# Optimization experiments

Measured on AMD Instinct MI355X. Metric: run time of the kernel, lower is better.

## Reference

```python
import jax, jax.numpy as jnp
import numpy as np

N_NODES = 100000
N_REL = 500
N_EDGES = 600000
DIM = 128


def setup_inputs() -> dict:
    key = jax.random.key(0)
    ks = jax.random.split(key, 10)
    ent = jax.random.normal(ks[0], (N_NODES, DIM), dtype=jnp.float32)
    rel = jax.random.normal(ks[1], (N_REL, DIM), dtype=jnp.float32)
    edge_index = jax.random.randint(ks[2], (2, N_EDGES), 0, N_NODES, dtype=jnp.int64)
    edge_type = jax.random.randint(ks[3], (N_EDGES,), 0, N_REL, dtype=jnp.int64)
    s = 1.0 / np.sqrt(DIM)
    W_self = jax.random.uniform(ks[4], (DIM, DIM), jnp.float32, -s, s)
    b_self = jax.random.uniform(ks[5], (DIM,), jnp.float32, -s, s)
    W_nei = jax.random.uniform(ks[6], (DIM, DIM), jnp.float32, -s, s)
    b_nei = jax.random.uniform(ks[7], (DIM,), jnp.float32, -s, s)
    W_rel = jax.random.uniform(ks[8], (DIM, DIM), jnp.float32, -s, s)
    b_rel = jax.random.uniform(ks[9], (DIM,), jnp.float32, -s, s)
    return {
        "ent": ent, "rel": rel, "edge_index": edge_index, "edge_type": edge_type,
        "W_self": W_self, "b_self": b_self,
        "W_nei": W_nei, "b_nei": b_nei,
        "W_rel": W_rel, "b_rel": b_rel,
    }


def reference(ent, rel, edge_index, edge_type, W_self, b_self, W_nei, b_nei, W_rel, b_rel):
    src, dst = edge_index[0], edge_index[1]
    # gather -> sigmoid-gate -> scatter-add
    msg = ent[src] * jax.nn.sigmoid(rel[edge_type])          # [E, dim]
    agg = jax.ops.segment_sum(msg, dst, num_segments=ent.shape[0])  # [N, dim]
    out_ent = jax.nn.relu(ent @ W_self.T + b_self + agg @ W_nei.T + b_nei)
    out_rel = rel @ W_rel.T + b_rel
    return (out_ent, out_rel)
```

## Files before the change

kernel.cpp:

```cpp
#include <hip/hip_runtime.h>
#include <hip/hip_bf16.h>
#include <math.h>

#define DIM 128

typedef __bf16 bf8 __attribute__((ext_vector_type(8)));
typedef float f4 __attribute__((ext_vector_type(4)));

struct __align__(8) bf16x4 { __hip_bfloat162 a, b; };

__global__ __launch_bounds__(256) void prep_kernel(
    const float* __restrict__ rel,
    const float* __restrict__ Ws,
    const float* __restrict__ Wn,
    const float* __restrict__ Wr,
    __hip_bfloat16* __restrict__ sigb,
    __hip_bfloat16* __restrict__ Wcat,
    float* __restrict__ Wt_rel,
    int* __restrict__ offs,
    int nSig, int sigBlocks, int N) {
    int b = blockIdx.x;
    if (b < sigBlocks) {
        int i = b * 256 + threadIdx.x;
        if (i < nSig) {
            float x = rel[i];
            sigb[i] = __float2bfloat16(1.0f / (1.0f + expf(-x)));
        }
    } else if (b < sigBlocks + 32) {
        int idx = (b - sigBlocks) * 256 + threadIdx.x;
        int j  = idx >> 6;
        int k0 = (idx & 63) * 4;
        const float* src = (k0 < DIM) ? &Ws[j * DIM + k0] : &Wn[j * DIM + (k0 - DIM)];
        float4 v = *(const float4*)src;
        bf16x4 o;
        o.a.x = __float2bfloat16(v.x);
        o.a.y = __float2bfloat16(v.y);
        o.b.x = __float2bfloat16(v.z);
        o.b.y = __float2bfloat16(v.w);
        *(bf16x4*)&Wcat[(size_t)j * 256 + k0] = o;
    } else if (b < sigBlocks + 32 + 64) {
        int id = (b - sigBlocks - 32) * 256 + threadIdx.x;
        int k = id >> 7;
        int j = id & 127;
        Wt_rel[id] = Wr[j * DIM + k];
    } else {
        int i = (b - sigBlocks - 32 - 64) * 256 + threadIdx.x;
        if (i <= N) offs[i] = 0;
    }
}

__global__ __launch_bounds__(256) void conv_hist_kernel(
    const float* __restrict__ ent,
    __hip_bfloat16* __restrict__ xcat,
    const int* __restrict__ edge_index,
    int* __restrict__ counts,
    int* __restrict__ rank,
    int N, int E, int convBlocks) {
    if ((int)blockIdx.x < convBlocks) {
        long long tid = (long long)blockIdx.x * 256 + threadIdx.x;
        int row = (int)(tid >> 5);
        int q   = (int)(tid & 31);
        if (row >= N) return;
        float4 v = *(const float4*)&ent[(size_t)row * DIM + q * 4];
        bf16x4 o;
        o.a.x = __float2bfloat16(v.x);
        o.a.y = __float2bfloat16(v.y);
        o.b.x = __float2bfloat16(v.z);
        o.b.y = __float2bfloat16(v.w);
        *(bf16x4*)&xcat[(size_t)row * 256 + q * 4] = o;
    } else {
        int e = (blockIdx.x - convBlocks) * 256 + threadIdx.x;
        if (e < E) {
            rank[e] = atomicAdd(&counts[edge_index[E + e]], 1);
        }
    }
}

#define SCAN_TPB 256
#define SCAN_IPT 4
#define SCAN_IPB 1024

__global__ void scan_pass1(int* __restrict__ data,
                           int* __restrict__ blockSums, int N) {
    __shared__ int ts[SCAN_TPB];
    int t = threadIdx.x;
    int base = blockIdx.x * SCAN_IPB + t * SCAN_IPT;
    int v[SCAN_IPT];
    int s = 0;
    #pragma unroll
    for (int i = 0; i < SCAN_IPT; ++i) {
        int idx = base + i;
        v[i] = (idx < N) ? data[idx] : 0;
        s += v[i];
    }
    ts[t] = s;
    __syncthreads();
    for (int off = 1; off < SCAN_TPB; off <<= 1) {
        int x = (t >= off) ? ts[t - off] : 0;
        __syncthreads();
        ts[t] += x;
        __syncthreads();
    }
    int excl = ts[t] - s;
    #pragma unroll
    for (int i = 0; i < SCAN_IPT; ++i) {
        int idx = base + i;
        if (idx < N) data[idx] = excl;
        excl += v[i];
    }
    if (t == SCAN_TPB - 1) blockSums[blockIdx.x] = ts[t];
}

__global__ __launch_bounds__(256) void scan_finish_kernel(
    int* __restrict__ offs, const int* __restrict__ blockSums,
    int nb, int N, int E) {
    __shared__ int ps[128];
    __shared__ int eps[128];
    int t = threadIdx.x;
    int v = 0;
    if (t < 128) {
        v = (t < nb) ? blockSums[t] : 0;
        ps[t] = v;
    }
    __syncthreads();
    for (int off = 1; off < 128; off <<= 1) {
        int x = (t >= off && t < 128) ? ps[t - off] : 0;
        __syncthreads();
        if (t < 128) ps[t] += x;
        __syncthreads();
    }
    if (t < 128) eps[t] = ps[t] - v;
    __syncthreads();
    int i = blockIdx.x * 256 + t;
    if (i < N)  offs[i] += eps[i >> 10];
    if (i == N) offs[N] = E;
}

__global__ void scatter_ids_kernel(const int* __restrict__ edge_index,
                                   const int* __restrict__ edge_type,
                                   const int* __restrict__ offs,
                                   const int* __restrict__ rank,
                                   unsigned* __restrict__ spack, int E) {
    int e = blockIdx.x * blockDim.x + threadIdx.x;
    if (e >= E) return;
    int dst = edge_index[E + e];
    int p = offs[dst] + rank[e];
    spack[p] = (unsigned)edge_index[e] | ((unsigned)edge_type[e] << 17);
}

__global__ __launch_bounds__(256) void agg_relout_kernel(
    const __hip_bfloat16* __restrict__ xcat,
    const __hip_bfloat16* __restrict__ sigb,
    const int* __restrict__ offs,
    const unsigned* __restrict__ spack,
    __hip_bfloat16* __restrict__ xcat_w,
    const float* __restrict__ rel,
    const float* __restrict__ Wt_rel,
    const float* __restrict__ b_rel,
    float* __restrict__ out_rel,
    int N, int R, int aggBlocks) {
    if ((int)blockIdx.x < aggBlocks) {
        int wid  = (int)((blockIdx.x * (long long)256 + threadIdx.x) >> 6);
        int lane = threadIdx.x & 63;
        if (wid >= N) return;
        int beg = offs[wid], end = offs[wid + 1];
        float ax0 = 0.f, ay0 = 0.f, ax1 = 0.f, ay1 = 0.f;
        for (int e = beg; e < end; e += 4) {
            int r = end - e;
            unsigned p0 = spack[e];
            unsigned p1 = spack[r > 1 ? e + 1 : e];
            unsigned p2 = spack[r > 2 ? e + 2 : e];
            unsigned p3 = spack[r > 3 ? e + 3 : e];
            __hip_bfloat162 v0 = *(const __hip_bfloat162*)&xcat[(size_t)(p0 & 0x1FFFFu) * 256 + lane * 2];
            __hip_bfloat162 v1 = *(const __hip_bfloat162*)&xcat[(size_t)(p1 & 0x1FFFFu) * 256 + lane * 2];
            __hip_bfloat162 v2 = *(const __hip_bfloat162*)&xcat[(size_t)(p2 & 0x1FFFFu) * 256 + lane * 2];
            __hip_bfloat162 v3 = *(const __hip_bfloat162*)&xcat[(size_t)(p3 & 0x1FFFFu) * 256 + lane * 2];
            __hip_bfloat162 g0 = *(const __hip_bfloat162*)&sigb[(size_t)(p0 >> 17) * DIM + lane * 2];
            __hip_bfloat162 g1 = *(const __hip_bfloat162*)&sigb[(size_t)(p1 >> 17) * DIM + lane * 2];
            __hip_bfloat162 g2 = *(const __hip_bfloat162*)&sigb[(size_t)(p2 >> 17) * DIM + lane * 2];
            __hip_bfloat162 g3 = *(const __hip_bfloat162*)&sigb[(size_t)(p3 >> 17) * DIM + lane * 2];
            float m1 = (r > 1) ? 1.f : 0.f;
            float m2 = (r > 2) ? 1.f : 0.f;
            float m3 = (r > 3) ? 1.f : 0.f;
            ax0 += __bfloat162float(v0.x) * __bfloat162float(g0.x);
            ay0 += __bfloat162float(v0.y) * __bfloat162float(g0.y);
            ax1 += m1 * (__bfloat162float(v1.x) * __bfloat162float(g1.x));
            ay1 += m1 * (__bfloat162float(v1.y) * __bfloat162float(g1.y));
            ax0 += m2 * (__bfloat162float(v2.x) * __bfloat162float(g2.x));
            ay0 += m2 * (__bfloat162float(v2.y) * __bfloat162float(g2.y));
            ax1 += m3 * (__bfloat162float(v3.x) * __bfloat162float(g3.x));
            ay1 += m3 * (__bfloat162float(v3.y) * __bfloat162float(g3.y));
        }
        __hip_bfloat162 o;
        o.x = __float2bfloat16(ax0 + ax1);
        o.y = __float2bfloat16(ay0 + ay1);
        *(__hip_bfloat162*)&xcat_w[(size_t)wid * 256 + 128 + lane * 2] = o;
    } else {
        __shared__ float rr[2][DIM];
        int idx  = blockIdx.x - aggBlocks;
        int half = threadIdx.x >> 7;
        int col  = threadIdx.x & 127;
        int row  = idx * 2 + half;
        if (row < R) rr[half][col] = rel[(size_t)row * DIM + col];
        __syncthreads();
        if (row >= R) return;
        float acc = b_rel[col];
        #pragma unroll 8
        for (int k = 0; k < DIM; ++k) {
            acc += rr[half][k] * Wt_rel[k * DIM + col];
        }
        out_rel[(size_t)row * DIM + col] = acc;
    }
}

__global__ __launch_bounds__(256) void gemm_mfma_kernel(
    const __hip_bfloat16* xcat,
    const __hip_bfloat16* __restrict__ Wcat,
    const float* __restrict__ b_self,
    const float* __restrict__ b_nei,
    float* out, int N) {
    __shared__ __hip_bfloat16 Bs[128][264];

    int t    = threadIdx.x;
    int wave = t >> 6;
    int lane = t & 63;
    int quad = lane >> 4;
    int r16  = lane & 15;

    {
        int r = t >> 1, h = t & 1;
        const float4* src = (const float4*)&Wcat[(size_t)r * 256 + h * 128];
        #pragma unroll
        for (int i = 0; i < 16; ++i) {
            *(float4*)&Bs[r][h * 128 + i * 8] = src[i];
        }
    }
    __syncthreads();

    int row0 = blockIdx.x * 128 + wave * 32;

    bf8 x[2][8];
    #pragma unroll
    for (int mt = 0; mt < 2; ++mt) {
        int m = row0 + mt * 16 + r16;
        if (m > N - 1) m = N - 1;
        const __hip_bfloat16* xp = &xcat[(size_t)m * 256 + quad * 8];
        #pragma unroll
        for (int ks = 0; ks < 8; ++ks) {
            x[mt][ks] = *(const bf8*)(xp + ks * 32);
        }
    }

    f4 acc[2][8];
    #pragma unroll
    for (int mt = 0; mt < 2; ++mt)
        #pragma unroll
        for (int jt = 0; jt < 8; ++jt)
            acc[mt][jt] = (f4){0.f, 0.f, 0.f, 0.f};

    #pragma unroll
    for (int ks = 0; ks < 8; ++ks) {
        #pragma unroll
        for (int jt = 0; jt < 8; ++jt) {
            bf8 w = *(const bf8*)&Bs[jt * 16 + r16][ks * 32 + quad * 8];
            acc[0][jt] = __builtin_amdgcn_mfma_f32_16x16x32_bf16(w, x[0][ks], acc[0][jt], 0, 0, 0);
            acc[1][jt] = __builtin_amdgcn_mfma_f32_16x16x32_bf16(w, x[1][ks], acc[1][jt], 0, 0, 0);
        }
    }

    f4 bias4[8];
    #pragma unroll
    for (int jt = 0; jt < 8; ++jt) {
        const float4 bs = *(const float4*)&b_self[jt * 16 + quad * 4];
        const float4 bn = *(const float4*)&b_nei[jt * 16 + quad * 4];
        bias4[jt] = (f4){bs.x + bn.x, bs.y + bn.y, bs.z + bn.z, bs.w + bn.w};
    }

    #pragma unroll
    for (int mt = 0; mt < 2; ++mt) {
        int m = row0 + mt * 16 + r16;
        if (m < N) {
            #pragma unroll
            for (int jt = 0; jt < 8; ++jt) {
                f4 v = acc[mt][jt] + bias4[jt];
                float4 o;
                o.x = fmaxf(v[0], 0.f);
                o.y = fmaxf(v[1], 0.f);
                o.z = fmaxf(v[2], 0.f);
                o.w = fmaxf(v[3], 0.f);
                *(float4*)&out[(size_t)m * DIM + jt * 16 + quad * 4] = o;
            }
        }
    }
}

extern "C" void kernel_launch(void* const* d_in, const int* in_sizes, int n_in,
                              void* d_out, int out_size, void* d_ws, size_t ws_size,
                              hipStream_t stream) {
    const float* ent        = (const float*)d_in[0];
    const float* rel        = (const float*)d_in[1];
    const int*   edge_index = (const int*)d_in[2];
    const int*   edge_type  = (const int*)d_in[3];
    const float* W_self     = (const float*)d_in[4];
    const float* b_self     = (const float*)d_in[5];
    const float* W_nei      = (const float*)d_in[6];
    const float* b_nei      = (const float*)d_in[7];
    const float* W_rel      = (const float*)d_in[8];
    const float* b_rel      = (const float*)d_in[9];

    const int N = in_sizes[0] / DIM;
    const int R = in_sizes[1] / DIM;
    const int E = in_sizes[3];

    float* out     = (float*)d_out;
    float* out_rel = out + (size_t)N * DIM;
    __hip_bfloat16* xcat = (__hip_bfloat16*)d_out;

    __hip_bfloat16* sigb = (__hip_bfloat16*)d_ws;
    float* Wt_rel  = (float*)(sigb + (size_t)R * DIM);
    __hip_bfloat16* Wcat = (__hip_bfloat16*)(Wt_rel + DIM * DIM);
    int*   offs    = (int*)(Wcat + 128 * 256);
    int*   bsums   = offs + (N + 8);
    int*   rank    = bsums + 128;
    unsigned* spack = (unsigned*)(rank + E);

    const int nSig = R * DIM;
    const int sigBlocks = (nSig + 255) / 256;
    const int zeroBlocks = (N + 1 + 255) / 256;
    const int scanBlocks = (N + SCAN_IPB - 1) / SCAN_IPB;

    prep_kernel<<<sigBlocks + 32 + 64 + zeroBlocks, 256, 0, stream>>>(
        rel, W_self, W_nei, W_rel, sigb, Wcat, Wt_rel, offs, nSig, sigBlocks, N);

    {
        int convBlocks = (int)(((long long)N * 32 + 255) / 256);
        int histBlocks = (E + 255) / 256;
        conv_hist_kernel<<<convBlocks + histBlocks, 256, 0, stream>>>(
            ent, xcat, edge_index, offs, rank, N, E, convBlocks);
    }

    scan_pass1<<<scanBlocks, SCAN_TPB, 0, stream>>>(offs, bsums, N);
    scan_finish_kernel<<<(N + 1 + 255) / 256, 256, 0, stream>>>(
        offs, bsums, scanBlocks, N, E);

    scatter_ids_kernel<<<(E + 255) / 256, 256, 0, stream>>>(
        edge_index, edge_type, offs, rank, spack, E);

    {
        int aggBlocks = (int)(((long long)N * 64 + 255) / 256);
        int relBlocks = (R + 1) / 2;
        agg_relout_kernel<<<aggBlocks + relBlocks, 256, 0, stream>>>(
            xcat, sigb, offs, spack, xcat, rel, Wt_rel, b_rel, out_rel,
            N, R, aggBlocks);
    }

    {
        int blocks = (N + 127) / 128;
        gemm_mfma_kernel<<<blocks, 256, 0, stream>>>(xcat, Wcat, b_self, b_nei, out, N);
    }
}
```

Before: 227.1 us.

## Split wavefront into two edge groups with vectorized index loads and fp32 gates

```diff
diff --git a/kernel.cpp b/kernel.cpp
--- a/kernel.cpp
+++ b/kernel.cpp
@@ -14,17 +14,21 @@
     const float* __restrict__ Ws,
     const float* __restrict__ Wn,
     const float* __restrict__ Wr,
-    __hip_bfloat16* __restrict__ sigb,
+    float* __restrict__ sigf,
     __hip_bfloat16* __restrict__ Wcat,
     float* __restrict__ Wt_rel,
     int* __restrict__ offs,
-    int nSig, int sigBlocks, int N) {
+    int nSig, int nSigTot, int sigBlocks, int N) {
     int b = blockIdx.x;
     if (b < sigBlocks) {
         int i = b * 256 + threadIdx.x;
-        if (i < nSig) {
-            float x = rel[i];
-            sigb[i] = __float2bfloat16(1.0f / (1.0f + expf(-x)));
+        if (i < nSigTot) {
+            float v = 0.f;
+            if (i < nSig) {
+                float x = rel[i];
+                v = 1.0f / (1.0f + expf(-x));
+            }
+            sigf[i] = v;
         }
     } else if (b < sigBlocks + 32) {
         int idx = (b - sigBlocks) * 256 + threadIdx.x;
@@ -150,7 +154,7 @@
 
 __global__ __launch_bounds__(256) void agg_relout_kernel(
     const __hip_bfloat16* __restrict__ xcat,
-    const __hip_bfloat16* __restrict__ sigb,
+    const float* __restrict__ sigf,
     const int* __restrict__ offs,
     const unsigned* __restrict__ spack,
     __hip_bfloat16* __restrict__ xcat_w,
@@ -163,38 +167,47 @@
         int wid  = (int)((blockIdx.x * (long long)256 + threadIdx.x) >> 6);
         int lane = threadIdx.x & 63;
         if (wid >= N) return;
+        int h = lane >> 5;
+        int s = lane & 31;
         int beg = offs[wid], end = offs[wid + 1];
-        float ax0 = 0.f, ay0 = 0.f, ax1 = 0.f, ay1 = 0.f;
-        for (int e = beg; e < end; e += 4) {
-            int r = end - e;
-            unsigned p0 = spack[e];
-            unsigned p1 = spack[r > 1 ? e + 1 : e];
-            unsigned p2 = spack[r > 2 ? e + 2 : e];
-            unsigned p3 = spack[r > 3 ? e + 3 : e];
-            __hip_bfloat162 v0 = *(const __hip_bfloat162*)&xcat[(size_t)(p0 & 0x1FFFFu) * 256 + lane * 2];
-            __hip_bfloat162 v1 = *(const __hip_bfloat162*)&xcat[(size_t)(p1 & 0x1FFFFu) * 256 + lane * 2];
-            __hip_bfloat162 v2 = *(const __hip_bfloat162*)&xcat[(size_t)(p2 & 0x1FFFFu) * 256 + lane * 2];
-            __hip_bfloat162 v3 = *(const __hip_bfloat162*)&xcat[(size_t)(p3 & 0x1FFFFu) * 256 + lane * 2];
-            __hip_bfloat162 g0 = *(const __hip_bfloat162*)&sigb[(size_t)(p0 >> 17) * DIM + lane * 2];
-            __hip_bfloat162 g1 = *(const __hip_bfloat162*)&sigb[(size_t)(p1 >> 17) * DIM + lane * 2];
-            __hip_bfloat162 g2 = *(const __hip_bfloat162*)&sigb[(size_t)(p2 >> 17) * DIM + lane * 2];
-            __hip_bfloat162 g3 = *(const __hip_bfloat162*)&sigb[(size_t)(p3 >> 17) * DIM + lane * 2];
-            float m1 = (r > 1) ? 1.f : 0.f;
-            float m2 = (r > 2) ? 1.f : 0.f;
-            float m3 = (r > 3) ? 1.f : 0.f;
-            ax0 += __bfloat162float(v0.x) * __bfloat162float(g0.x);
-            ay0 += __bfloat162float(v0.y) * __bfloat162float(g0.y);
-            ax1 += m1 * (__bfloat162float(v1.x) * __bfloat162float(g1.x));
-            ay1 += m1 * (__bfloat162float(v1.y) * __bfloat162float(g1.y));
-            ax0 += m2 * (__bfloat162float(v2.x) * __bfloat162float(g2.x));
-            ay0 += m2 * (__bfloat162float(v2.y) * __bfloat162float(g2.y));
-            ax1 += m3 * (__bfloat162float(v3.x) * __bfloat162float(g3.x));
-            ay1 += m3 * (__bfloat162float(v3.y) * __bfloat162float(g3.y));
-        }
-        __hip_bfloat162 o;
-        o.x = __float2bfloat16(ax0 + ax1);
-        o.y = __float2bfloat16(ay0 + ay1);
-        *(__hip_bfloat162*)&xcat_w[(size_t)wid * 256 + 128 + lane * 2] = o;
+        unsigned len = (unsigned)(end - beg);
+        const unsigned SENT = ((unsigned)R) << 17;
+        unsigned so8  = (unsigned)s * 8;
+        unsigned so16 = (unsigned)s * 16;
+        float a0 = 0.f, a1 = 0.f, a2 = 0.f, a3 = 0.f;
+        int e0 = beg & ~3;
+        for (int e = e0; e < end; e += 8) {
+            int i0 = e + 4 * h;
+            uint4 pp = *(const uint4*)&spack[i0];
+            unsigned o0 = (unsigned)(i0 - beg);
+            unsigned p0 = (o0     < len) ? pp.x : SENT;
+            unsigned p1 = (o0 + 1 < len) ? pp.y : SENT;
+            unsigned p2 = (o0 + 2 < len) ? pp.z : SENT;
+            unsigned p3 = (o0 + 3 < len) ? pp.w : SENT;
+            #define EDGE(pj) { \
+                unsigned rb = (pj & 0x1FFFFu) << 9; \
+                unsigned tb = (pj >> 17) << 9; \
+                bf16x4 v = *(const bf16x4*)((const char*)xcat + rb + so8); \
+                float4 g = *(const float4*)((const char*)sigf + tb + so16); \
+                a0 += __bfloat162float(v.a.x) * g.x; \
+                a1 += __bfloat162float(v.a.y) * g.y; \
+                a2 += __bfloat162float(v.b.x) * g.z; \
+                a3 += __bfloat162float(v.b.y) * g.w; }
+            EDGE(p0); EDGE(p1); EDGE(p2); EDGE(p3);
+            #undef EDGE
+        }
+        a0 += __shfl_xor(a0, 32);
+        a1 += __shfl_xor(a1, 32);
+        a2 += __shfl_xor(a2, 32);
+        a3 += __shfl_xor(a3, 32);
+        if (h == 0) {
+            bf16x4 o;
+            o.a.x = __float2bfloat16(a0);
+            o.a.y = __float2bfloat16(a1);
+            o.b.x = __float2bfloat16(a2);
+            o.b.y = __float2bfloat16(a3);
+            *(bf16x4*)&xcat_w[(size_t)wid * 256 + 128 + s * 4] = o;
+        }
     } else {
         __shared__ float rr[2][DIM];
         int idx  = blockIdx.x - aggBlocks;
@@ -316,21 +329,23 @@
     float* out_rel = out + (size_t)N * DIM;
     __hip_bfloat16* xcat = (__hip_bfloat16*)d_out;
 
-    __hip_bfloat16* sigb = (__hip_bfloat16*)d_ws;
-    float* Wt_rel  = (float*)(sigb + (size_t)R * DIM);
+    float* sigf = (float*)d_ws;
+    float* Wt_rel  = sigf + (size_t)(R + 1) * DIM;
     __hip_bfloat16* Wcat = (__hip_bfloat16*)(Wt_rel + DIM * DIM);
     int*   offs    = (int*)(Wcat + 128 * 256);
     int*   bsums   = offs + (N + 8);
     int*   rank    = bsums + 128;
-    unsigned* spack = (unsigned*)(rank + E);
+    unsigned* spackAll = (unsigned*)(rank + E);
+    unsigned* spack = spackAll + 8;
 
     const int nSig = R * DIM;
-    const int sigBlocks = (nSig + 255) / 256;
+    const int nSigTot = (R + 1) * DIM;
+    const int sigBlocks = (nSigTot + 255) / 256;
     const int zeroBlocks = (N + 1 + 255) / 256;
     const int scanBlocks = (N + SCAN_IPB - 1) / SCAN_IPB;
 
     prep_kernel<<<sigBlocks + 32 + 64 + zeroBlocks, 256, 0, stream>>>(
-        rel, W_self, W_nei, W_rel, sigb, Wcat, Wt_rel, offs, nSig, sigBlocks, N);
+        rel, W_self, W_nei, W_rel, sigf, Wcat, Wt_rel, offs, nSig, nSigTot, sigBlocks, N);
 
     {
         int convBlocks = (int)(((long long)N * 32 + 255) / 256);
@@ -350,7 +365,7 @@
         int aggBlocks = (int)(((long long)N * 64 + 255) / 256);
         int relBlocks = (R + 1) / 2;
         agg_relout_kernel<<<aggBlocks + relBlocks, 256, 0, stream>>>(
-            xcat, sigb, offs, spack, xcat, rel, Wt_rel, b_rel, out_rel,
+            xcat, sigf, offs, spack, xcat, rel, Wt_rel, b_rel, out_rel,
             N, R, aggBlocks);
     }
 
```

Measured after the change: 233.3 us. +2.7%, slower.

## Pad CSR segments to multiples of four with precomputed byte offsets

Applied to the files above, without the earlier changes.

```diff
diff --git a/kernel.cpp b/kernel.cpp
--- a/kernel.cpp
+++ b/kernel.cpp
@@ -6,6 +6,7 @@
 
 typedef __bf16 bf8 __attribute__((ext_vector_type(8)));
 typedef float f4 __attribute__((ext_vector_type(4)));
+typedef float f2 __attribute__((ext_vector_type(2)));
 
 struct __align__(8) bf16x4 { __hip_bfloat162 a, b; };
 
@@ -18,13 +19,19 @@
     __hip_bfloat16* __restrict__ Wcat,
     float* __restrict__ Wt_rel,
     int* __restrict__ offs,
-    int nSig, int sigBlocks, int N) {
+    uint2* __restrict__ spack2,
+    int nSig, int nSigTot, int sigBlocks, int N, int R,
+    int zeroBlocks, int fillQuads) {
     int b = blockIdx.x;
     if (b < sigBlocks) {
         int i = b * 256 + threadIdx.x;
-        if (i < nSig) {
-            float x = rel[i];
-            sigb[i] = __float2bfloat16(1.0f / (1.0f + expf(-x)));
+        if (i < nSigTot) {
+            float v = 0.f;
+            if (i < nSig) {
+                float x = rel[i];
+                v = 1.0f / (1.0f + expf(-x));
+            }
+            sigb[i] = __float2bfloat16(v);
         }
     } else if (b < sigBlocks + 32) {
         int idx = (b - sigBlocks) * 256 + threadIdx.x;
@@ -43,9 +50,16 @@
         int k = id >> 7;
         int j = id & 127;
         Wt_rel[id] = Wr[j * DIM + k];
-    } else {
+    } else if (b < sigBlocks + 32 + 64 + zeroBlocks) {
         int i = (b - sigBlocks - 32 - 64) * 256 + threadIdx.x;
         if (i <= N) offs[i] = 0;
+    } else {
+        int i = (b - sigBlocks - 32 - 64 - zeroBlocks) * 256 + threadIdx.x;
+        if (i < fillQuads) {
+            unsigned gz = (unsigned)R * 256u;
+            uint4 s; s.x = 0u; s.y = gz; s.z = 0u; s.w = gz;
+            ((uint4*)spack2)[i] = s;
+        }
     }
 }
 
@@ -90,7 +104,8 @@
     #pragma unroll
     for (int i = 0; i < SCAN_IPT; ++i) {
         int idx = base + i;
-        v[i] = (idx < N) ? data[idx] : 0;
+        int c = (idx < N) ? data[idx] : 0;
+        v[i] = (c + 3) & ~3;
         s += v[i];
     }
     ts[t] = s;
@@ -113,7 +128,7 @@
 
 __global__ __launch_bounds__(256) void scan_finish_kernel(
     int* __restrict__ offs, const int* __restrict__ blockSums,
-    int nb, int N, int E) {
+    int nb, int N) {
     __shared__ int ps[128];
     __shared__ int eps[128];
     int t = threadIdx.x;
@@ -133,26 +148,29 @@
     __syncthreads();
     int i = blockIdx.x * 256 + t;
     if (i < N)  offs[i] += eps[i >> 10];
-    if (i == N) offs[N] = E;
+    if (i == N) offs[N] = ps[127];
 }
 
 __global__ void scatter_ids_kernel(const int* __restrict__ edge_index,
                                    const int* __restrict__ edge_type,
                                    const int* __restrict__ offs,
                                    const int* __restrict__ rank,
-                                   unsigned* __restrict__ spack, int E) {
+                                   uint2* __restrict__ spack2, int E) {
     int e = blockIdx.x * blockDim.x + threadIdx.x;
     if (e >= E) return;
     int dst = edge_index[E + e];
     int p = offs[dst] + rank[e];
-    spack[p] = (unsigned)edge_index[e] | ((unsigned)edge_type[e] << 17);
+    uint2 w;
+    w.x = (unsigned)edge_index[e] << 9;
+    w.y = (unsigned)edge_type[e] << 8;
+    spack2[p] = w;
 }
 
 __global__ __launch_bounds__(256) void agg_relout_kernel(
     const __hip_bfloat16* __restrict__ xcat,
     const __hip_bfloat16* __restrict__ sigb,
     const int* __restrict__ offs,
-    const unsigned* __restrict__ spack,
+    const uint2* __restrict__ spack2,
     __hip_bfloat16* __restrict__ xcat_w,
     const float* __restrict__ rel,
     const float* __restrict__ Wt_rel,
@@ -163,37 +181,41 @@
         int wid  = (int)((blockIdx.x * (long long)256 + threadIdx.x) >> 6);
         int lane = threadIdx.x & 63;
         if (wid >= N) return;
-        int beg = offs[wid], end = offs[wid + 1];
-        float ax0 = 0.f, ay0 = 0.f, ax1 = 0.f, ay1 = 0.f;
+        int beg = __builtin_amdgcn_readfirstlane(offs[wid]);
+        int end = __builtin_amdgcn_readfirstlane(offs[wid + 1]);
+        const char* xb = (const char*)xcat;
+        const char* gb = (const char*)sigb;
+        unsigned so = (unsigned)lane * 4;
+        f2 accA = (f2){0.f, 0.f};
+        f2 accB = (f2){0.f, 0.f};
         for (int e = beg; e < end; e += 4) {
-            int r = end - e;
-            unsigned p0 = spack[e];
-            unsigned p1 = spack[r > 1 ? e + 1 : e];
-            unsigned p2 = spack[r > 2 ? e + 2 : e];
-            unsigned p3 = spack[r > 3 ? e + 3 : e];
-            __hip_bfloat162 v0 = *(const __hip_bfloat162*)&xcat[(size_t)(p0 & 0x1FFFFu) * 256 + lane * 2];
-            __hip_bfloat162 v1 = *(const __hip_bfloat162*)&xcat[(size_t)(p1 & 0x1FFFFu) * 256 + lane * 2];
-            __hip_bfloat162 v2 = *(const __hip_bfloat162*)&xcat[(size_t)(p2 & 0x1FFFFu) * 256 + lane * 2];
-            __hip_bfloat162 v3 = *(const __hip_bfloat162*)&xcat[(size_t)(p3 & 0x1FFFFu) * 256 + lane * 2];
-            __hip_bfloat162 g0 = *(const __hip_bfloat162*)&sigb[(size_t)(p0 >> 17) * DIM + lane * 2];
-            __hip_bfloat162 g1 = *(const __hip_bfloat162*)&sigb[(size_t)(p1 >> 17) * DIM + lane * 2];
-            __hip_bfloat162 g2 = *(const __hip_bfloat162*)&sigb[(size_t)(p2 >> 17) * DIM + lane * 2];
-            __hip_bfloat162 g3 = *(const __hip_bfloat162*)&sigb[(size_t)(p3 >> 17) * DIM + lane * 2];
-            float m1 = (r > 1) ? 1.f : 0.f;
-            float m2 = (r > 2) ? 1.f : 0.f;
-            float m3 = (r > 3) ? 1.f : 0.f;
-            ax0 += __bfloat162float(v0.x) * __bfloat162float(g0.x);
-            ay0 += __bfloat162float(v0.y) * __bfloat162float(g0.y);
-            ax1 += m1 * (__bfloat162float(v1.x) * __bfloat162float(g1.x));
-            ay1 += m1 * (__bfloat162float(v1.y) * __bfloat162float(g1.y));
-            ax0 += m2 * (__bfloat162float(v2.x) * __bfloat162float(g2.x));
-            ay0 += m2 * (__bfloat162float(v2.y) * __bfloat162float(g2.y));
-            ax1 += m3 * (__bfloat162float(v3.x) * __bfloat162float(g3.x));
-            ay1 += m3 * (__bfloat162float(v3.y) * __bfloat162float(g3.y));
-        }
+            uint4 q01 = *(const uint4*)(spack2 + e);
+            uint4 q23 = *(const uint4*)(spack2 + e + 2);
+            __hip_bfloat162 v0 = *(const __hip_bfloat162*)(xb + (q01.x + so));
+            __hip_bfloat162 g0 = *(const __hip_bfloat162*)(gb + (q01.y + so));
+            __hip_bfloat162 v1 = *(const __hip_bfloat162*)(xb + (q01.z + so));
+            __hip_bfloat162 g1 = *(const __hip_bfloat162*)(gb + (q01.w + so));
+            __hip_bfloat162 v2 = *(const __hip_bfloat162*)(xb + (q23.x + so));
+            __hip_bfloat162 g2 = *(const __hip_bfloat162*)(gb + (q23.y + so));
+            __hip_bfloat162 v3 = *(const __hip_bfloat162*)(xb + (q23.z + so));
+            __hip_bfloat162 g3 = *(const __hip_bfloat162*)(gb + (q23.w + so));
+            f2 vf0 = (f2){__bfloat162float(v0.x), __bfloat162float(v0.y)};
+            f2 gf0 = (f2){__bfloat162float(g0.x), __bfloat162float(g0.y)};
+            f2 vf1 = (f2){__bfloat162float(v1.x), __bfloat162float(v1.y)};
+            f2 gf1 = (f2){__bfloat162float(g1.x), __bfloat162float(g1.y)};
+            f2 vf2 = (f2){__bfloat162float(v2.x), __bfloat162float(v2.y)};
+            f2 gf2 = (f2){__bfloat162float(g2.x), __bfloat162float(g2.y)};
+            f2 vf3 = (f2){__bfloat162float(v3.x), __bfloat162float(v3.y)};
+            f2 gf3 = (f2){__bfloat162float(g3.x), __bfloat162float(g3.y)};
+            accA += vf0 * gf0;
+            accB += vf1 * gf1;
+            accA += vf2 * gf2;
+            accB += vf3 * gf3;
+        }
+        f2 s = accA + accB;
         __hip_bfloat162 o;
-        o.x = __float2bfloat16(ax0 + ax1);
-        o.y = __float2bfloat16(ay0 + ay1);
+        o.x = __float2bfloat16(s.x);
+        o.y = __float2bfloat16(s.y);
         *(__hip_bfloat162*)&xcat_w[(size_t)wid * 256 + 128 + lane * 2] = o;
     } else {
         __shared__ float rr[2][DIM];
@@ -317,20 +339,24 @@
     __hip_bfloat16* xcat = (__hip_bfloat16*)d_out;
 
     __hip_bfloat16* sigb = (__hip_bfloat16*)d_ws;
-    float* Wt_rel  = (float*)(sigb + (size_t)R * DIM);
+    float* Wt_rel  = (float*)(sigb + (size_t)(R + 1) * DIM);
     __hip_bfloat16* Wcat = (__hip_bfloat16*)(Wt_rel + DIM * DIM);
     int*   offs    = (int*)(Wcat + 128 * 256);
     int*   bsums   = offs + (N + 8);
     int*   rank    = bsums + 128;
-    unsigned* spack = (unsigned*)(rank + E);
+    uint2* spack2  = (uint2*)(rank + E);
 
     const int nSig = R * DIM;
-    const int sigBlocks = (nSig + 255) / 256;
+    const int nSigTot = (R + 1) * DIM;
+    const int sigBlocks = (nSigTot + 255) / 256;
     const int zeroBlocks = (N + 1 + 255) / 256;
+    const int fillQuads = (E + 3 * N) / 2 + 8;
+    const int fillBlocks = (fillQuads + 255) / 256;
     const int scanBlocks = (N + SCAN_IPB - 1) / SCAN_IPB;
 
-    prep_kernel<<<sigBlocks + 32 + 64 + zeroBlocks, 256, 0, stream>>>(
-        rel, W_self, W_nei, W_rel, sigb, Wcat, Wt_rel, offs, nSig, sigBlocks, N);
+    prep_kernel<<<sigBlocks + 32 + 64 + zeroBlocks + fillBlocks, 256, 0, stream>>>(
+        rel, W_self, W_nei, W_rel, sigb, Wcat, Wt_rel, offs, spack2,
+        nSig, nSigTot, sigBlocks, N, R, zeroBlocks, fillQuads);
 
     {
         int convBlocks = (int)(((long long)N * 32 + 255) / 256);
@@ -341,16 +367,16 @@
 
     scan_pass1<<<scanBlocks, SCAN_TPB, 0, stream>>>(offs, bsums, N);
     scan_finish_kernel<<<(N + 1 + 255) / 256, 256, 0, stream>>>(
-        offs, bsums, scanBlocks, N, E);
+        offs, bsums, scanBlocks, N);
 
     scatter_ids_kernel<<<(E + 255) / 256, 256, 0, stream>>>(
-        edge_index, edge_type, offs, rank, spack, E);
+        edge_index, edge_type, offs, rank, spack2, E);
 
     {
         int aggBlocks = (int)(((long long)N * 64 + 255) / 256);
         int relBlocks = (R + 1) / 2;
         agg_relout_kernel<<<aggBlocks + relBlocks, 256, 0, stream>>>(
-            xcat, sigb, offs, spack, xcat, rel, Wt_rel, b_rel, out_rel,
+            xcat, sigb, offs, spack2, xcat, rel, Wt_rel, b_rel, out_rel,
             N, R, aggBlocks);
     }
 
```

Result: faster. 221.3 us (-2.6%).
